# Performance work log

Hardware: AMD Instinct MI355X
Metric: run time of the kernel (lower is better)

The kernel has to match this reference:

```python
import jax, jax.numpy as jnp
import numpy as np

N = 50000   # nodes
E = 600000  # edges
D = 128     # emb_dim
L = 5       # num_layers
ATOM_DIMS = np.array([119, 4, 11, 13, 11, 7, 13, 2, 9]) + 5   # per-feature vocab (+5 as in source)
BOND_DIMS = np.array([7, 22, 2]) + 5
BL_CENTERS = np.arange(0.0, 2.0, 0.1, dtype=np.float32)   # 20 centers, gamma 10
PR_CENTERS = np.arange(0.0, 1.0, 0.05, dtype=np.float32)  # 20 centers, gamma 1
BL_GAMMA = 10.0
PR_GAMMA = 1.0
BN_EPS = 1e-5


def setup_inputs() -> dict:
    key = jax.random.key(0)
    ks = jax.random.split(key, 16)
    scale = 1.0 / np.sqrt(D)
    atom_off = jnp.asarray(np.concatenate([[0], np.cumsum(ATOM_DIMS)[:-1]]), jnp.int32)
    bond_off = jnp.asarray(np.concatenate([[0], np.cumsum(BOND_DIMS)[:-1]]), jnp.int32)
    return {
        "x": jax.random.randint(ks[0], (N, 9), 0, 7, dtype=jnp.int32),
        "edge_index": jax.random.randint(ks[1], (2, E), 0, N, dtype=jnp.int32),
        "edge_attr_int": jax.random.randint(ks[2], (E, 3), 0, 7, dtype=jnp.int32),
        "edge_attr_float": jax.random.uniform(ks[3], (E, 2), dtype=jnp.float32),
        "atom_off": atom_off,
        "bond_off": bond_off,
        "atom_emb": jax.random.normal(ks[4], (int(ATOM_DIMS.sum()), D), jnp.float32) * scale,
        "bond_emb": jax.random.normal(ks[5], (L, int(BOND_DIMS.sum()), D), jnp.float32) * scale,
        "W_bl": jax.random.normal(ks[6], (L, len(BL_CENTERS), D), jnp.float32) * scale,
        "b_bl": jnp.zeros((L, D), jnp.float32),
        "W_pr": jax.random.normal(ks[7], (L, len(PR_CENTERS), D), jnp.float32) * scale,
        "b_pr": jnp.zeros((L, D), jnp.float32),
        "mlp_W1": jax.random.normal(ks[8], (L, D, D), jnp.float32) * scale,
        "mlp_b1": jnp.zeros((L, D), jnp.float32),
        "bn1_g": jnp.ones((L, D), jnp.float32),
        "bn1_b": jnp.zeros((L, D), jnp.float32),
        "mlp_W2": jax.random.normal(ks[9], (L, D, D), jnp.float32) * scale,
        "mlp_b2": jnp.zeros((L, D), jnp.float32),
        "eps_gin": jnp.zeros((L,), jnp.float32),
        "bn_g": jnp.ones((L, D), jnp.float32),
        "bn_b": jnp.zeros((L, D), jnp.float32),
    }


def _bn(h, g, b):
    # BatchNorm1d, training-mode batch statistics over the node axis
    m = h.mean(0)
    v = h.var(0)
    return (h - m) * jax.lax.rsqrt(v + BN_EPS) * g + b


def _rbf(x, centers, gamma):
    # exp(-gamma * (x - c)^2): [E] -> [E, n_centers]
    return jnp.exp(-gamma * jnp.square(x[:, None] - centers[None, :]))


def reference(x, edge_index, edge_attr_int, edge_attr_float, atom_off, bond_off,
              atom_emb, bond_emb, W_bl, b_bl, W_pr, b_pr,
              mlp_W1, mlp_b1, bn1_g, bn1_b, mlp_W2, mlp_b2,
              eps_gin, bn_g, bn_b):
    # AtomEncoder: sum of 9 categorical embeddings (flat table + offsets)
    h = atom_emb[x + atom_off[None, :]].sum(1)  # [N, D]
    src, dst = edge_index[0], edge_index[1]
    bl = _rbf(edge_attr_float[:, 0], jnp.asarray(BL_CENTERS), BL_GAMMA)  # [E, 20]
    pr = _rbf(edge_attr_float[:, 1], jnp.asarray(PR_CENTERS), PR_GAMMA)  # [E, 20]
    for l in range(L):
        # per-layer edge embedding: BondEncoder + BondFloatRBF
        e = bond_emb[l][edge_attr_int + bond_off[None, :]].sum(1)
        e = e + bl @ W_bl[l] + b_bl[l] + pr @ W_pr[l] + b_pr[l]
        # GINConv (aggr='add'): mlp((1+eps)*x + sum_j relu(x_j + e_ij))
        msg = jax.nn.relu(h[src] + e)                       # [E, D]
        agg = jax.ops.segment_sum(msg, dst, num_segments=N)  # [N, D]
        z = (1.0 + eps_gin[l]) * h + agg
        z = z @ mlp_W1[l] + mlp_b1[l]
        z = jax.nn.relu(_bn(z, bn1_g[l], bn1_b[l]))
        z = z @ mlp_W2[l] + mlp_b2[l]
        # outer per-layer BatchNorm; ReLU except last layer (drop_ratio=0)
        z = _bn(z, bn_g[l], bn_b[l])
        if l < L - 1:
            z = jax.nn.relu(z)
        h = z
    return h  # JK='last'
```

## Files before the change

### kernel.cpp

```cpp
#include <hip/hip_runtime.h>
#include <hip/hip_bf16.h>

#define GN 50000
#define GE 600000
#define DD 128
#define TQ 4096
#define NBOND 2268
#define TROWS (2*(TQ+1) + NBOND)
#define SCB 49
#define NBANK 16
#define SSET (NBANK*256)
#define NB 782

typedef __attribute__((ext_vector_type(8))) short short8;
typedef __attribute__((ext_vector_type(4))) float floatx4;

__device__ __forceinline__ unsigned short f2b(float f) {
    __hip_bfloat16 h = __float2bfloat16(f);
    return __builtin_bit_cast(unsigned short, h);
}
__device__ __forceinline__ float b2f_lo(unsigned int u) { return __uint_as_float(u << 16); }
__device__ __forceinline__ float b2f_hi(unsigned int u) { return __uint_as_float(u & 0xffff0000u); }
__device__ __forceinline__ float bs2f(short s) {
    return __uint_as_float(((unsigned int)(unsigned short)s) << 16);
}

__global__ __launch_bounds__(256) void atom_kernel(
    const int* __restrict__ x, const int* __restrict__ atom_off,
    const float* __restrict__ atom_emb, unsigned short* __restrict__ h)
{
    int t = blockIdx.x * 256 + threadIdx.x;
    if (t >= GN * DD) return;
    int n = t >> 7, d = t & 127;
    float s = 0.f;
#pragma unroll
    for (int f = 0; f < 9; f++) {
        int idx = x[n * 9 + f] + atom_off[f];
        s += atom_emb[idx * DD + d];
    }
    h[t] = f2b(s);
}

__global__ __launch_bounds__(256) void hist_kernel(const int* __restrict__ ei, int* __restrict__ count)
{
    int e = blockIdx.x * 256 + threadIdx.x;
    if (e < GE) atomicAdd(&count[ei[GE + e]], 1);
}

__global__ __launch_bounds__(1024) void scan1_kernel(
    const int* __restrict__ count, int* __restrict__ row_start, int* __restrict__ blocksum)
{
    __shared__ int sh[1024];
    int t = threadIdx.x;
    int idx = blockIdx.x * 1024 + t;
    int v = (idx < GN) ? count[idx] : 0;
    sh[t] = v;
    __syncthreads();
    for (int off = 1; off < 1024; off <<= 1) {
        int u = (t >= off) ? sh[t - off] : 0;
        __syncthreads();
        sh[t] += u;
        __syncthreads();
    }
    if (idx <= GN) row_start[idx] = (t == 0) ? 0 : sh[t - 1];
    if (t == 1023) blocksum[blockIdx.x] = sh[1023];
}

__global__ __launch_bounds__(64) void scan2_kernel(
    const int* __restrict__ blocksum, int* __restrict__ blockoff)
{
    int t = threadIdx.x;
    int v = (t < SCB) ? blocksum[t] : 0;
#pragma unroll
    for (int off = 1; off < 64; off <<= 1) {
        int u = __shfl_up(v, off);
        if (t >= off) v += u;
    }
    int e = __shfl_up(v, 1);
    if (t == 0) e = 0;
    if (t < SCB) blockoff[t] = e;
}

__global__ __launch_bounds__(1024) void scan3_kernel(
    int* __restrict__ row_start, const int* __restrict__ blockoff)
{
    int idx = blockIdx.x * 1024 + threadIdx.x;
    if (idx <= GN) row_start[idx] += blockoff[blockIdx.x];
}

__global__ __launch_bounds__(256) void scatter_kernel(
    const int* __restrict__ ei, const int* __restrict__ eai, const float* __restrict__ eaf,
    const int* __restrict__ row_start, int* __restrict__ fill, int4* __restrict__ ep)
{
    int e = blockIdx.x * 256 + threadIdx.x;
    if (e < GE) {
        int d = ei[GE + e];
        int p = row_start[d] + atomicAdd(&fill[d], 1);
        int src = ei[e];
        float x1 = eaf[2 * e], x2 = eaf[2 * e + 1];
        int q1 = (int)(x1 * (float)TQ + 0.5f); q1 = min(max(q1, 0), TQ);
        int q2 = (int)(x2 * (float)TQ + 0.5f); q2 = min(max(q2, 0), TQ);
        int b0 = eai[3 * e], b1 = eai[3 * e + 1], b2 = eai[3 * e + 2];
        ep[p] = make_int4(src, q1 | (q2 << 16), (b0 * 27 + b1) * 7 + b2, 0);
    }
}

__global__ __launch_bounds__(128) void tables_kernel(
    const float* __restrict__ W_bl, const float* __restrict__ b_bl,
    const float* __restrict__ W_pr, const float* __restrict__ b_pr,
    const float* __restrict__ bond_emb, const int* __restrict__ bond_off,
    unsigned short* __restrict__ tbl_bl, unsigned short* __restrict__ tbl_pr,
    unsigned short* __restrict__ tbl_bond)
{
    int l = blockIdx.x / TROWS;
    int b = blockIdx.x % TROWS;
    int d = threadIdx.x;
    const float* W_bl_l = W_bl + (size_t)l * 20 * DD;
    const float* W_pr_l = W_pr + (size_t)l * 20 * DD;
    const float* bemb_l = bond_emb + (size_t)l * 46 * DD;
    if (b < (TQ + 1)) {
        float xq = b * (1.0f / TQ);
        float s = b_bl[(size_t)l * DD + d] + b_pr[(size_t)l * DD + d];
#pragma unroll
        for (int k = 0; k < 20; k++) {
            float dl = xq - 0.1f * k;
            s += __expf(-10.f * dl * dl) * W_bl_l[k * DD + d];
        }
        tbl_bl[((size_t)l * (TQ + 1) + b) * DD + d] = f2b(s);
    } else if (b < 2 * (TQ + 1)) {
        int q = b - (TQ + 1);
        float xq = q * (1.0f / TQ);
        float s = 0.f;
#pragma unroll
        for (int k = 0; k < 20; k++) {
            float dl = xq - 0.05f * k;
            s += __expf(-dl * dl) * W_pr_l[k * DD + d];
        }
        tbl_pr[((size_t)l * (TQ + 1) + q) * DD + d] = f2b(s);
    } else {
        int r = b - 2 * (TQ + 1);
        int b0 = r / 189;
        int rem = r % 189;
        int b1 = rem / 7, b2 = rem % 7;
        tbl_bond[((size_t)l * NBOND + r) * DD + d] =
            f2b(bemb_l[(b0 + bond_off[0]) * DD + d]
              + bemb_l[(b1 + bond_off[1]) * DD + d]
              + bemb_l[(b2 + bond_off[2]) * DD + d]);
    }
}

__global__ __launch_bounds__(256) void wfrag_kernel(
    const float* __restrict__ W1, const float* __restrict__ W2,
    unsigned short* __restrict__ wf_hi, unsigned short* __restrict__ wf_lo)
{
    int t = blockIdx.x * 256 + threadIdx.x;
    if (t >= 10 * 2048) return;
    int mat = t >> 11;
    int rem = t & 2047;
    int kt = rem >> 9;
    int rem2 = rem & 511;
    int nt = rem2 >> 6;
    int lane = rem2 & 63;
    const float* src = (mat & 1) ? (W2 + (size_t)(mat >> 1) * DD * DD)
                                 : (W1 + (size_t)(mat >> 1) * DD * DD);
    int n = nt * 16 + (lane & 15);
    int k0 = kt * 32 + (lane >> 4) * 8;
    size_t base = (size_t)mat * 16384 + (size_t)((kt * 8 + nt) * 64 + lane) * 8;
#pragma unroll
    for (int j = 0; j < 8; j++) {
        float w = src[(size_t)(k0 + j) * DD + n];
        unsigned short hi = f2b(w);
        wf_hi[base + j] = hi;
        wf_lo[base + j] = f2b(w - bs2f((short)hi));
    }
}

__global__ __launch_bounds__(256) void edge_kernel(
    const int4* __restrict__ ep,
    const unsigned short* __restrict__ tbl_bl, const unsigned short* __restrict__ tbl_pr,
    const unsigned short* __restrict__ tbl_bond,
    const unsigned short* __restrict__ hsrc, const int* __restrict__ row_start,
    const float* __restrict__ eps_gin, int layer, int apply_bn,
    const float* __restrict__ stats_prev, const float* __restrict__ g_prev,
    const float* __restrict__ b_prev,
    float* __restrict__ A)
{
    __shared__ float sc_s[DD], tr_s[DD];
    int tid = threadIdx.x;
    if (tid < DD) {
        float sc = 1.f, tr = 0.f;
        if (apply_bn) {
            float s = 0.f, q = 0.f;
#pragma unroll
            for (int bk = 0; bk < NBANK; bk++) {
                s += stats_prev[bk * 256 + tid];
                q += stats_prev[bk * 256 + 128 + tid];
            }
            float m = s * (1.0f / GN);
            float v = q * (1.0f / GN) - m * m;
            sc = g_prev[tid] * rsqrtf(v + 1e-5f);
            tr = b_prev[tid] - m * sc;
        }
        sc_s[tid] = sc;
        tr_s[tid] = tr;
    }
    __syncthreads();

    int wid = __builtin_amdgcn_readfirstlane(tid >> 6);
    int lane = tid & 63;
    float sc0 = sc_s[2 * lane],     tr0 = tr_s[2 * lane];
    float sc1 = sc_s[2 * lane + 1], tr1 = tr_s[2 * lane + 1];
    float rmin = apply_bn ? 0.f : -__builtin_inff();

    int n = blockIdx.x * 4 + wid;
    int s0 = __builtin_amdgcn_readfirstlane(row_start[n]);
    int s1 = __builtin_amdgcn_readfirstlane(row_start[n + 1]);
    const unsigned int* hu = (const unsigned int*)hsrc;
    const unsigned int* tb = (const unsigned int*)tbl_bl;
    const unsigned int* tp = (const unsigned int*)tbl_pr;
    const unsigned int* tg = (const unsigned int*)tbl_bond;
    float a0 = 0.f, a1 = 0.f;
    int p = s0;
    for (; p + 2 <= s1; p += 2) {
        int4 m0 = ep[p];
        int4 m1 = ep[p + 1];
        unsigned int ub0 = tb[(size_t)(m0.y & 0xffff) * 64 + lane];
        unsigned int up0 = tp[(size_t)((unsigned)m0.y >> 16) * 64 + lane];
        unsigned int ug0 = tg[(size_t)m0.z * 64 + lane];
        unsigned int uh0 = hu[(size_t)m0.x * 64 + lane];
        unsigned int ub1 = tb[(size_t)(m1.y & 0xffff) * 64 + lane];
        unsigned int up1 = tp[(size_t)((unsigned)m1.y >> 16) * 64 + lane];
        unsigned int ug1 = tg[(size_t)m1.z * 64 + lane];
        unsigned int uh1 = hu[(size_t)m1.x * 64 + lane];
        float h00 = fmaxf(fmaf(b2f_lo(uh0), sc0, tr0), rmin);
        float h01 = fmaxf(fmaf(b2f_hi(uh0), sc1, tr1), rmin);
        float h10 = fmaxf(fmaf(b2f_lo(uh1), sc0, tr0), rmin);
        float h11 = fmaxf(fmaf(b2f_hi(uh1), sc1, tr1), rmin);
        a0 += fmaxf(h00 + b2f_lo(ub0) + b2f_lo(up0) + b2f_lo(ug0), 0.f);
        a1 += fmaxf(h01 + b2f_hi(ub0) + b2f_hi(up0) + b2f_hi(ug0), 0.f);
        a0 += fmaxf(h10 + b2f_lo(ub1) + b2f_lo(up1) + b2f_lo(ug1), 0.f);
        a1 += fmaxf(h11 + b2f_hi(ub1) + b2f_hi(up1) + b2f_hi(ug1), 0.f);
    }
    if (p < s1) {
        int4 m0 = ep[p];
        unsigned int ub0 = tb[(size_t)(m0.y & 0xffff) * 64 + lane];
        unsigned int up0 = tp[(size_t)((unsigned)m0.y >> 16) * 64 + lane];
        unsigned int ug0 = tg[(size_t)m0.z * 64 + lane];
        unsigned int uh0 = hu[(size_t)m0.x * 64 + lane];
        float h00 = fmaxf(fmaf(b2f_lo(uh0), sc0, tr0), rmin);
        float h01 = fmaxf(fmaf(b2f_hi(uh0), sc1, tr1), rmin);
        a0 += fmaxf(h00 + b2f_lo(ub0) + b2f_lo(up0) + b2f_lo(ug0), 0.f);
        a1 += fmaxf(h01 + b2f_hi(ub0) + b2f_hi(up0) + b2f_hi(ug0), 0.f);
    }
    float eps1 = 1.f + eps_gin[layer];
    unsigned int un = hu[(size_t)n * 64 + lane];
    a0 += eps1 * fmaxf(fmaf(b2f_lo(un), sc0, tr0), rmin);
    a1 += eps1 * fmaxf(fmaf(b2f_hi(un), sc1, tr1), rmin);
    float2 o; o.x = a0; o.y = a1;
    *(float2*)(A + (size_t)n * DD + 2 * lane) = o;
}

__global__ __launch_bounds__(256) void gemm1_kernel(
    const float* __restrict__ Asrc,
    const unsigned short* __restrict__ wf_hi, const unsigned short* __restrict__ wf_lo,
    const float* __restrict__ bias, float* __restrict__ Cdst, float* __restrict__ stats_out)
{
    __shared__ float red_s[4][DD];
    __shared__ float red_q[4][DD];
    int tid = threadIdx.x, wid = tid >> 6, lane = tid & 63;
    int quad = lane >> 4, l16 = lane & 15;
    int row = blockIdx.x * 64 + wid * 16 + l16;
    bool rvalid = row < GN;

    floatx4 acc[8];
#pragma unroll
    for (int nt = 0; nt < 8; nt++) acc[nt] = (floatx4){0.f, 0.f, 0.f, 0.f};

    const short8* bhp = (const short8*)wf_hi;
    const short8* blp = (const short8*)wf_lo;
#pragma unroll
    for (int kt = 0; kt < 4; kt++) {
        short8 ahi = {0,0,0,0,0,0,0,0}, alo = {0,0,0,0,0,0,0,0};
        if (rvalid) {
            const float* ap = Asrc + (size_t)row * DD + kt * 32 + quad * 8;
            float a[8];
            *(float4*)(a)     = *(const float4*)(ap);
            *(float4*)(a + 4) = *(const float4*)(ap + 4);
#pragma unroll
            for (int j = 0; j < 8; j++) {
                unsigned short hi = f2b(a[j]);
                ahi[j] = (short)hi;
                alo[j] = (short)f2b(a[j] - bs2f((short)hi));
            }
        }
#pragma unroll
        for (int nt = 0; nt < 8; nt++) {
            short8 bhi = bhp[(kt * 8 + nt) * 64 + lane];
            short8 blo = blp[(kt * 8 + nt) * 64 + lane];
            acc[nt] = __builtin_amdgcn_mfma_f32_16x16x32_bf16(ahi, bhi, acc[nt], 0, 0, 0);
            acc[nt] = __builtin_amdgcn_mfma_f32_16x16x32_bf16(alo, bhi, acc[nt], 0, 0, 0);
            acc[nt] = __builtin_amdgcn_mfma_f32_16x16x32_bf16(ahi, blo, acc[nt], 0, 0, 0);
        }
    }

#pragma unroll
    for (int nt = 0; nt < 8; nt++) {
        int col = nt * 16 + l16;
        float bv = bias[col];
        float s = 0.f, q = 0.f;
#pragma unroll
        for (int v = 0; v < 4; v++) {
            int r = blockIdx.x * 64 + wid * 16 + quad * 4 + v;
            float o = acc[nt][v] + bv;
            if (r < GN) {
                s += o; q += o * o;
                Cdst[(size_t)r * DD + col] = o;
            }
        }
        s += __shfl_xor(s, 16); s += __shfl_xor(s, 32);
        q += __shfl_xor(q, 16); q += __shfl_xor(q, 32);
        if (lane < 16) { red_s[wid][col] = s; red_q[wid][col] = q; }
    }
    __syncthreads();
    int bank = blockIdx.x & (NBANK - 1);
    if (tid < DD) {
        float s = red_s[0][tid] + red_s[1][tid] + red_s[2][tid] + red_s[3][tid];
        atomicAdd(&stats_out[bank * 256 + tid], s);
    } else {
        int c = tid - DD;
        float q = red_q[0][c] + red_q[1][c] + red_q[2][c] + red_q[3][c];
        atomicAdd(&stats_out[bank * 256 + 128 + c], q);
    }
}

__global__ __launch_bounds__(256) void gemm2_kernel(
    const float* __restrict__ Asrc,
    const unsigned short* __restrict__ wf_hi, const unsigned short* __restrict__ wf_lo,
    const float* __restrict__ bias,
    unsigned short* __restrict__ Cbf, float* __restrict__ Cf32, int out_bf16,
    const float* __restrict__ stats_in, const float* __restrict__ bn_g,
    const float* __restrict__ bn_b, float* __restrict__ stats_out)
{
    __shared__ float sc_s[DD], tr_s[DD];
    __shared__ float red_s[4][DD];
    __shared__ float red_q[4][DD];
    int tid = threadIdx.x, wid = tid >> 6, lane = tid & 63;
    if (tid < DD) {
        float s = 0.f, q = 0.f;
#pragma unroll
        for (int bk = 0; bk < NBANK; bk++) {
            s += stats_in[bk * 256 + tid];
            q += stats_in[bk * 256 + 128 + tid];
        }
        float m = s * (1.0f / GN);
        float v = q * (1.0f / GN) - m * m;
        float sc = bn_g[tid] * rsqrtf(v + 1e-5f);
        sc_s[tid] = sc;
        tr_s[tid] = bn_b[tid] - m * sc;
    }
    __syncthreads();
    int quad = lane >> 4, l16 = lane & 15;
    int row = blockIdx.x * 64 + wid * 16 + l16;
    bool rvalid = row < GN;

    floatx4 acc[8];
#pragma unroll
    for (int nt = 0; nt < 8; nt++) acc[nt] = (floatx4){0.f, 0.f, 0.f, 0.f};

    const short8* bhp = (const short8*)wf_hi;
    const short8* blp = (const short8*)wf_lo;
#pragma unroll
    for (int kt = 0; kt < 4; kt++) {
        short8 ahi = {0,0,0,0,0,0,0,0}, alo = {0,0,0,0,0,0,0,0};
        if (rvalid) {
            const float* ap = Asrc + (size_t)row * DD + kt * 32 + quad * 8;
            float a[8];
            *(float4*)(a)     = *(const float4*)(ap);
            *(float4*)(a + 4) = *(const float4*)(ap + 4);
            int kb = kt * 32 + quad * 8;
#pragma unroll
            for (int j = 0; j < 8; j++)
                a[j] = fmaxf(a[j] * sc_s[kb + j] + tr_s[kb + j], 0.f);
#pragma unroll
            for (int j = 0; j < 8; j++) {
                unsigned short hi = f2b(a[j]);
                ahi[j] = (short)hi;
                alo[j] = (short)f2b(a[j] - bs2f((short)hi));
            }
        }
#pragma unroll
        for (int nt = 0; nt < 8; nt++) {
            short8 bhi = bhp[(kt * 8 + nt) * 64 + lane];
            short8 blo = blp[(kt * 8 + nt) * 64 + lane];
            acc[nt] = __builtin_amdgcn_mfma_f32_16x16x32_bf16(ahi, bhi, acc[nt], 0, 0, 0);
            acc[nt] = __builtin_amdgcn_mfma_f32_16x16x32_bf16(alo, bhi, acc[nt], 0, 0, 0);
            acc[nt] = __builtin_amdgcn_mfma_f32_16x16x32_bf16(ahi, blo, acc[nt], 0, 0, 0);
        }
    }

#pragma unroll
    for (int nt = 0; nt < 8; nt++) {
        int col = nt * 16 + l16;
        float bv = bias[col];
        float s = 0.f, q = 0.f;
#pragma unroll
        for (int v = 0; v < 4; v++) {
            int r = blockIdx.x * 64 + wid * 16 + quad * 4 + v;
            float o = acc[nt][v] + bv;
            if (r < GN) {
                s += o; q += o * o;
                if (out_bf16) Cbf[(size_t)r * DD + col] = f2b(o);
                else          Cf32[(size_t)r * DD + col] = o;
            }
        }
        s += __shfl_xor(s, 16); s += __shfl_xor(s, 32);
        q += __shfl_xor(q, 16); q += __shfl_xor(q, 32);
        if (lane < 16) { red_s[wid][col] = s; red_q[wid][col] = q; }
    }
    __syncthreads();
    int bank = blockIdx.x & (NBANK - 1);
    if (tid < DD) {
        float s = red_s[0][tid] + red_s[1][tid] + red_s[2][tid] + red_s[3][tid];
        atomicAdd(&stats_out[bank * 256 + tid], s);
    } else {
        int c = tid - DD;
        float q = red_q[0][c] + red_q[1][c] + red_q[2][c] + red_q[3][c];
        atomicAdd(&stats_out[bank * 256 + 128 + c], q);
    }
}

__global__ __launch_bounds__(256) void bn_apply_kernel(
    const float* __restrict__ Z, const float* __restrict__ stats2,
    const float* __restrict__ g, const float* __restrict__ b,
    float* __restrict__ fout)
{
    __shared__ float sc_s[DD], tr_s[DD];
    int tid = threadIdx.x;
    if (tid < DD) {
        float s = 0.f, q = 0.f;
#pragma unroll
        for (int bk = 0; bk < NBANK; bk++) {
            s += stats2[bk * 256 + tid];
            q += stats2[bk * 256 + 128 + tid];
        }
        float m = s * (1.0f / GN);
        float v = q * (1.0f / GN) - m * m;
        float sc = g[tid] * rsqrtf(v + 1e-5f);
        sc_s[tid] = sc;
        tr_s[tid] = b[tid] - m * sc;
    }
    __syncthreads();
    const int total = GN * DD;
    for (int t = blockIdx.x * 256 + tid; t < total; t += gridDim.x * 256) {
        int c = t & 127;
        fout[t] = Z[t] * sc_s[c] + tr_s[c];
    }
}

extern "C" void kernel_launch(void* const* d_in, const int* in_sizes, int n_in,
                              void* d_out, int out_size, void* d_ws, size_t ws_size,
                              hipStream_t stream)
{
    const int*   x        = (const int*)d_in[0];
    const int*   ei       = (const int*)d_in[1];
    const int*   eai      = (const int*)d_in[2];
    const float* eaf      = (const float*)d_in[3];
    const int*   atom_off = (const int*)d_in[4];
    const int*   bond_off = (const int*)d_in[5];
    const float* atom_emb = (const float*)d_in[6];
    const float* bond_emb = (const float*)d_in[7];
    const float* W_bl     = (const float*)d_in[8];
    const float* b_bl     = (const float*)d_in[9];
    const float* W_pr     = (const float*)d_in[10];
    const float* b_pr     = (const float*)d_in[11];
    const float* W1       = (const float*)d_in[12];
    const float* b1       = (const float*)d_in[13];
    const float* bn1g     = (const float*)d_in[14];
    const float* bn1b     = (const float*)d_in[15];
    const float* W2       = (const float*)d_in[16];
    const float* b2       = (const float*)d_in[17];
    const float* eps_gin  = (const float*)d_in[18];
    const float* bng      = (const float*)d_in[19];
    const float* bnb      = (const float*)d_in[20];
    float* out = (float*)d_out;

    char* p = (char*)d_ws;
    unsigned short* h_bf  = (unsigned short*)p;  p += (size_t)GN * DD * 2;
    unsigned short* z2_bf = (unsigned short*)p;  p += (size_t)GN * DD * 2;
    float* A              = (float*)p;           p += (size_t)GN * DD * 4;
    float* z1             = (float*)p;           p += (size_t)GN * DD * 4;
    float* z2f            = (float*)p;           p += (size_t)GN * DD * 4;
    unsigned short* tbl_bl   = (unsigned short*)p;  p += (size_t)5 * (TQ + 1) * DD * 2;
    unsigned short* tbl_pr   = (unsigned short*)p;  p += (size_t)5 * (TQ + 1) * DD * 2;
    unsigned short* tbl_bond = (unsigned short*)p;  p += (size_t)5 * NBOND * DD * 2;
    unsigned short* wf_hi    = (unsigned short*)p;  p += (size_t)10 * 16384 * 2;
    unsigned short* wf_lo    = (unsigned short*)p;  p += (size_t)10 * 16384 * 2;
    float* stats_all = (float*)p;  p += (size_t)10 * SSET * 4;
    int* count    = (int*)p;    p += (size_t)GN * 4;
    int* fill     = (int*)p;    p += (size_t)GN * 4;
    int* row_start= (int*)p;    p += (size_t)(GN + 1) * 4;
    int* blocksum = (int*)p;    p += (size_t)SCB * 4;
    int* blockoff = (int*)p;    p += (size_t)SCB * 4;
    p = (char*)(((size_t)p + 15) & ~(size_t)15);
    int4* ep      = (int4*)p;   p += (size_t)GE * 16;

    hipMemsetAsync(count, 0, (size_t)GN * 4, stream);
    hipMemsetAsync(fill,  0, (size_t)GN * 4, stream);
    hipMemsetAsync(stats_all, 0, (size_t)10 * SSET * 4, stream);

    hist_kernel<<<(GE + 255) / 256, 256, 0, stream>>>(ei, count);
    scan1_kernel<<<SCB, 1024, 0, stream>>>(count, row_start, blocksum);
    scan2_kernel<<<1, 64, 0, stream>>>(blocksum, blockoff);
    scan3_kernel<<<SCB, 1024, 0, stream>>>(row_start, blockoff);
    scatter_kernel<<<(GE + 255) / 256, 256, 0, stream>>>(ei, eai, eaf, row_start, fill, ep);
    atom_kernel<<<(GN * DD + 255) / 256, 256, 0, stream>>>(x, atom_off, atom_emb, h_bf);
    wfrag_kernel<<<80, 256, 0, stream>>>(W1, W2, wf_hi, wf_lo);
    tables_kernel<<<5 * TROWS, 128, 0, stream>>>(
        W_bl, b_bl, W_pr, b_pr, bond_emb, bond_off, tbl_bl, tbl_pr, tbl_bond);

    for (int l = 0; l < 5; l++) {
        float* stats1 = stats_all + (size_t)(2 * l + 0) * SSET;
        float* stats2 = stats_all + (size_t)(2 * l + 1) * SSET;
        float* stats2_prev = stats_all + (size_t)(2 * (l - 1) + 1) * SSET;

        edge_kernel<<<GN / 4, 256, 0, stream>>>(
            ep,
            tbl_bl + (size_t)l * (TQ + 1) * DD,
            tbl_pr + (size_t)l * (TQ + 1) * DD,
            tbl_bond + (size_t)l * NBOND * DD,
            (l == 0) ? h_bf : z2_bf, row_start, eps_gin, l,
            (l > 0) ? 1 : 0,
            (l > 0) ? stats2_prev : stats_all,
            bng + (size_t)(l > 0 ? l - 1 : 0) * DD,
            bnb + (size_t)(l > 0 ? l - 1 : 0) * DD,
            A);

        gemm1_kernel<<<NB, 256, 0, stream>>>(
            A, wf_hi + (size_t)(l * 2 + 0) * 16384, wf_lo + (size_t)(l * 2 + 0) * 16384,
            b1 + (size_t)l * DD, z1, stats1);

        gemm2_kernel<<<NB, 256, 0, stream>>>(
            z1, wf_hi + (size_t)(l * 2 + 1) * 16384, wf_lo + (size_t)(l * 2 + 1) * 16384,
            b2 + (size_t)l * DD,
            z2_bf, z2f, (l < 4) ? 1 : 0,
            stats1, bn1g + (size_t)l * DD, bn1b + (size_t)l * DD, stats2);
    }

    bn_apply_kernel<<<1024, 256, 0, stream>>>(
        z2f, stats_all + (size_t)9 * SSET, bng + (size_t)4 * DD, bnb + (size_t)4 * DD, out);
}
```

Baseline: 742.8 us.

## Split GEMM kernels across four column tiles to raise block count

Both MLP GEMM kernels now split the 128 output columns into four 32-column tiles, each handled by its own block, which quadruples the grid from 782 to 3128 blocks. The goal is more parallelism and fewer accumulator registers per thread, so occupancy rises and the 256 CUs are better filled. The cost is that every block re-reads and re-converts the same A rows to bf16 hi/lo, so A traffic and conversion work grow fourfold (mostly served from L2), and gemm2 recomputes the BN scale/shift in every block.

```diff
diff --git a/kernel.cpp b/kernel.cpp
--- a/kernel.cpp
+++ b/kernel.cpp
@@ -11,6 +11,7 @@
 #define NBANK 16
 #define SSET (NBANK*256)
 #define NB 782
+#define NB4 (NB*4)
 
 typedef __attribute__((ext_vector_type(8))) short short8;
 typedef __attribute__((ext_vector_type(4))) float floatx4;
@@ -265,16 +266,19 @@
     const unsigned short* __restrict__ wf_hi, const unsigned short* __restrict__ wf_lo,
     const float* __restrict__ bias, float* __restrict__ Cdst, float* __restrict__ stats_out)
 {
-    __shared__ float red_s[4][DD];
-    __shared__ float red_q[4][DD];
+    __shared__ float red_s[4][32];
+    __shared__ float red_q[4][32];
     int tid = threadIdx.x, wid = tid >> 6, lane = tid & 63;
+    int ct = blockIdx.x & 3;
+    int rb = blockIdx.x >> 2;
+    int row0 = rb * 64;
     int quad = lane >> 4, l16 = lane & 15;
-    int row = blockIdx.x * 64 + wid * 16 + l16;
+    int row = row0 + wid * 16 + l16;
     bool rvalid = row < GN;
 
-    floatx4 acc[8];
-#pragma unroll
-    for (int nt = 0; nt < 8; nt++) acc[nt] = (floatx4){0.f, 0.f, 0.f, 0.f};
+    floatx4 acc[2];
+    acc[0] = (floatx4){0.f, 0.f, 0.f, 0.f};
+    acc[1] = (floatx4){0.f, 0.f, 0.f, 0.f};
 
     const short8* bhp = (const short8*)wf_hi;
     const short8* blp = (const short8*)wf_lo;
@@ -294,9 +298,10 @@
             }
         }
 #pragma unroll
-        for (int nt = 0; nt < 8; nt++) {
-            short8 bhi = bhp[(kt * 8 + nt) * 64 + lane];
-            short8 blo = blp[(kt * 8 + nt) * 64 + lane];
+        for (int nt = 0; nt < 2; nt++) {
+            int ntg = ct * 2 + nt;
+            short8 bhi = bhp[(kt * 8 + ntg) * 64 + lane];
+            short8 blo = blp[(kt * 8 + ntg) * 64 + lane];
             acc[nt] = __builtin_amdgcn_mfma_f32_16x16x32_bf16(ahi, bhi, acc[nt], 0, 0, 0);
             acc[nt] = __builtin_amdgcn_mfma_f32_16x16x32_bf16(alo, bhi, acc[nt], 0, 0, 0);
             acc[nt] = __builtin_amdgcn_mfma_f32_16x16x32_bf16(ahi, blo, acc[nt], 0, 0, 0);
@@ -304,13 +309,13 @@
     }
 
 #pragma unroll
-    for (int nt = 0; nt < 8; nt++) {
-        int col = nt * 16 + l16;
+    for (int nt = 0; nt < 2; nt++) {
+        int col = (ct * 2 + nt) * 16 + l16;
         float bv = bias[col];
         float s = 0.f, q = 0.f;
 #pragma unroll
         for (int v = 0; v < 4; v++) {
-            int r = blockIdx.x * 64 + wid * 16 + quad * 4 + v;
+            int r = row0 + wid * 16 + quad * 4 + v;
             float o = acc[nt][v] + bv;
             if (r < GN) {
                 s += o; q += o * o;
@@ -319,17 +324,18 @@
         }
         s += __shfl_xor(s, 16); s += __shfl_xor(s, 32);
         q += __shfl_xor(q, 16); q += __shfl_xor(q, 32);
-        if (lane < 16) { red_s[wid][col] = s; red_q[wid][col] = q; }
+        if (lane < 16) { red_s[wid][nt * 16 + lane] = s; red_q[wid][nt * 16 + lane] = q; }
     }
     __syncthreads();
-    int bank = blockIdx.x & (NBANK - 1);
-    if (tid < DD) {
+    int bank = (blockIdx.x >> 2) & (NBANK - 1);
+    int c0 = ct * 32;
+    if (tid < 32) {
         float s = red_s[0][tid] + red_s[1][tid] + red_s[2][tid] + red_s[3][tid];
-        atomicAdd(&stats_out[bank * 256 + tid], s);
-    } else {
-        int c = tid - DD;
+        atomicAdd(&stats_out[bank * 256 + c0 + tid], s);
+    } else if (tid < 64) {
+        int c = tid - 32;
         float q = red_q[0][c] + red_q[1][c] + red_q[2][c] + red_q[3][c];
-        atomicAdd(&stats_out[bank * 256 + 128 + c], q);
+        atomicAdd(&stats_out[bank * 256 + 128 + c0 + c], q);
     }
 }
 
@@ -342,8 +348,8 @@
     const float* __restrict__ bn_b, float* __restrict__ stats_out)
 {
     __shared__ float sc_s[DD], tr_s[DD];
-    __shared__ float red_s[4][DD];
-    __shared__ float red_q[4][DD];
+    __shared__ float red_s[4][32];
+    __shared__ float red_q[4][32];
     int tid = threadIdx.x, wid = tid >> 6, lane = tid & 63;
     if (tid < DD) {
         float s = 0.f, q = 0.f;
@@ -359,13 +365,16 @@
         tr_s[tid] = bn_b[tid] - m * sc;
     }
     __syncthreads();
+    int ct = blockIdx.x & 3;
+    int rb = blockIdx.x >> 2;
+    int row0 = rb * 64;
     int quad = lane >> 4, l16 = lane & 15;
-    int row = blockIdx.x * 64 + wid * 16 + l16;
+    int row = row0 + wid * 16 + l16;
     bool rvalid = row < GN;
 
-    floatx4 acc[8];
-#pragma unroll
-    for (int nt = 0; nt < 8; nt++) acc[nt] = (floatx4){0.f, 0.f, 0.f, 0.f};
+    floatx4 acc[2];
+    acc[0] = (floatx4){0.f, 0.f, 0.f, 0.f};
+    acc[1] = (floatx4){0.f, 0.f, 0.f, 0.f};
 
     const short8* bhp = (const short8*)wf_hi;
     const short8* blp = (const short8*)wf_lo;
@@ -389,9 +398,10 @@
             }
         }
 #pragma unroll
-        for (int nt = 0; nt < 8; nt++) {
-            short8 bhi = bhp[(kt * 8 + nt) * 64 + lane];
-            short8 blo = blp[(kt * 8 + nt) * 64 + lane];
+        for (int nt = 0; nt < 2; nt++) {
+            int ntg = ct * 2 + nt;
+            short8 bhi = bhp[(kt * 8 + ntg) * 64 + lane];
+            short8 blo = blp[(kt * 8 + ntg) * 64 + lane];
             acc[nt] = __builtin_amdgcn_mfma_f32_16x16x32_bf16(ahi, bhi, acc[nt], 0, 0, 0);
             acc[nt] = __builtin_amdgcn_mfma_f32_16x16x32_bf16(alo, bhi, acc[nt], 0, 0, 0);
             acc[nt] = __builtin_amdgcn_mfma_f32_16x16x32_bf16(ahi, blo, acc[nt], 0, 0, 0);
@@ -399,13 +409,13 @@
     }
 
 #pragma unroll
-    for (int nt = 0; nt < 8; nt++) {
-        int col = nt * 16 + l16;
+    for (int nt = 0; nt < 2; nt++) {
+        int col = (ct * 2 + nt) * 16 + l16;
         float bv = bias[col];
         float s = 0.f, q = 0.f;
 #pragma unroll
         for (int v = 0; v < 4; v++) {
-            int r = blockIdx.x * 64 + wid * 16 + quad * 4 + v;
+            int r = row0 + wid * 16 + quad * 4 + v;
             float o = acc[nt][v] + bv;
             if (r < GN) {
                 s += o; q += o * o;
@@ -415,17 +425,18 @@
         }
         s += __shfl_xor(s, 16); s += __shfl_xor(s, 32);
         q += __shfl_xor(q, 16); q += __shfl_xor(q, 32);
-        if (lane < 16) { red_s[wid][col] = s; red_q[wid][col] = q; }
+        if (lane < 16) { red_s[wid][nt * 16 + lane] = s; red_q[wid][nt * 16 + lane] = q; }
     }
     __syncthreads();
-    int bank = blockIdx.x & (NBANK - 1);
-    if (tid < DD) {
+    int bank = (blockIdx.x >> 2) & (NBANK - 1);
+    int c0 = ct * 32;
+    if (tid < 32) {
         float s = red_s[0][tid] + red_s[1][tid] + red_s[2][tid] + red_s[3][tid];
-        atomicAdd(&stats_out[bank * 256 + tid], s);
-    } else {
-        int c = tid - DD;
+        atomicAdd(&stats_out[bank * 256 + c0 + tid], s);
+    } else if (tid < 64) {
+        int c = tid - 32;
         float q = red_q[0][c] + red_q[1][c] + red_q[2][c] + red_q[3][c];
-        atomicAdd(&stats_out[bank * 256 + 128 + c], q);
+        atomicAdd(&stats_out[bank * 256 + 128 + c0 + c], q);
     }
 }
 
@@ -535,11 +546,11 @@
             bnb + (size_t)(l > 0 ? l - 1 : 0) * DD,
             A);
 
-        gemm1_kernel<<<NB, 256, 0, stream>>>(
+        gemm1_kernel<<<NB4, 256, 0, stream>>>(
             A, wf_hi + (size_t)(l * 2 + 0) * 16384, wf_lo + (size_t)(l * 2 + 0) * 16384,
             b1 + (size_t)l * DD, z1, stats1);
 
-        gemm2_kernel<<<NB, 256, 0, stream>>>(
+        gemm2_kernel<<<NB4, 256, 0, stream>>>(
             z1, wf_hi + (size_t)(l * 2 + 1) * 16384, wf_lo + (size_t)(l * 2 + 1) * 16384,
             b2 + (size_t)l * DD,
             z2_bf, z2f, (l < 4) ? 1 : 0,
```

Result: no change. 747.8 us (+0.7%).

## Stage GEMM A tile in LDS and split output columns across waves

Applied to the files above, without the earlier changes.

The two MLP GEMM kernels are merged into one template. Each block now loads its 64-row A tile into padded shared memory with coalesced float4 loads. Each wave then computes all 64 rows for 2 of the 8 column tiles, so each wave fetches a quarter of the hi/lo weight fragments it fetched before, and the A rows are reused across its MFMAs. The per-block shared reduction of BN statistics is replaced by per-wave atomics straight into the banked stats buffer. The cost is 4x more global atomics, an extra LDS round trip, and an unguarded tile load that reads past row N in the last block.

```diff
diff --git a/kernel.cpp b/kernel.cpp
--- a/kernel.cpp
+++ b/kernel.cpp
@@ -11,6 +11,7 @@
 #define NBANK 16
 #define SSET (NBANK*256)
 #define NB 782
+#define LDA2 132
 
 typedef __attribute__((ext_vector_type(8))) short short8;
 typedef __attribute__((ext_vector_type(4))) float floatx4;
@@ -260,80 +261,8 @@
     *(float2*)(A + (size_t)n * DD + 2 * lane) = o;
 }
 
-__global__ __launch_bounds__(256) void gemm1_kernel(
-    const float* __restrict__ Asrc,
-    const unsigned short* __restrict__ wf_hi, const unsigned short* __restrict__ wf_lo,
-    const float* __restrict__ bias, float* __restrict__ Cdst, float* __restrict__ stats_out)
-{
-    __shared__ float red_s[4][DD];
-    __shared__ float red_q[4][DD];
-    int tid = threadIdx.x, wid = tid >> 6, lane = tid & 63;
-    int quad = lane >> 4, l16 = lane & 15;
-    int row = blockIdx.x * 64 + wid * 16 + l16;
-    bool rvalid = row < GN;
-
-    floatx4 acc[8];
-#pragma unroll
-    for (int nt = 0; nt < 8; nt++) acc[nt] = (floatx4){0.f, 0.f, 0.f, 0.f};
-
-    const short8* bhp = (const short8*)wf_hi;
-    const short8* blp = (const short8*)wf_lo;
-#pragma unroll
-    for (int kt = 0; kt < 4; kt++) {
-        short8 ahi = {0,0,0,0,0,0,0,0}, alo = {0,0,0,0,0,0,0,0};
-        if (rvalid) {
-            const float* ap = Asrc + (size_t)row * DD + kt * 32 + quad * 8;
-            float a[8];
-            *(float4*)(a)     = *(const float4*)(ap);
-            *(float4*)(a + 4) = *(const float4*)(ap + 4);
-#pragma unroll
-            for (int j = 0; j < 8; j++) {
-                unsigned short hi = f2b(a[j]);
-                ahi[j] = (short)hi;
-                alo[j] = (short)f2b(a[j] - bs2f((short)hi));
-            }
-        }
-#pragma unroll
-        for (int nt = 0; nt < 8; nt++) {
-            short8 bhi = bhp[(kt * 8 + nt) * 64 + lane];
-            short8 blo = blp[(kt * 8 + nt) * 64 + lane];
-            acc[nt] = __builtin_amdgcn_mfma_f32_16x16x32_bf16(ahi, bhi, acc[nt], 0, 0, 0);
-            acc[nt] = __builtin_amdgcn_mfma_f32_16x16x32_bf16(alo, bhi, acc[nt], 0, 0, 0);
-            acc[nt] = __builtin_amdgcn_mfma_f32_16x16x32_bf16(ahi, blo, acc[nt], 0, 0, 0);
-        }
-    }
-
-#pragma unroll
-    for (int nt = 0; nt < 8; nt++) {
-        int col = nt * 16 + l16;
-        float bv = bias[col];
-        float s = 0.f, q = 0.f;
-#pragma unroll
-        for (int v = 0; v < 4; v++) {
-            int r = blockIdx.x * 64 + wid * 16 + quad * 4 + v;
-            float o = acc[nt][v] + bv;
-            if (r < GN) {
-                s += o; q += o * o;
-                Cdst[(size_t)r * DD + col] = o;
-            }
-        }
-        s += __shfl_xor(s, 16); s += __shfl_xor(s, 32);
-        q += __shfl_xor(q, 16); q += __shfl_xor(q, 32);
-        if (lane < 16) { red_s[wid][col] = s; red_q[wid][col] = q; }
-    }
-    __syncthreads();
-    int bank = blockIdx.x & (NBANK - 1);
-    if (tid < DD) {
-        float s = red_s[0][tid] + red_s[1][tid] + red_s[2][tid] + red_s[3][tid];
-        atomicAdd(&stats_out[bank * 256 + tid], s);
-    } else {
-        int c = tid - DD;
-        float q = red_q[0][c] + red_q[1][c] + red_q[2][c] + red_q[3][c];
-        atomicAdd(&stats_out[bank * 256 + 128 + c], q);
-    }
-}
-
-__global__ __launch_bounds__(256) void gemm2_kernel(
+template <int MODE>
+__global__ __launch_bounds__(256) void gemm_kernel(
     const float* __restrict__ Asrc,
     const unsigned short* __restrict__ wf_hi, const unsigned short* __restrict__ wf_lo,
     const float* __restrict__ bias,
@@ -341,91 +270,109 @@
     const float* __restrict__ stats_in, const float* __restrict__ bn_g,
     const float* __restrict__ bn_b, float* __restrict__ stats_out)
 {
+    __shared__ float At[64 * LDA2];
     __shared__ float sc_s[DD], tr_s[DD];
-    __shared__ float red_s[4][DD];
-    __shared__ float red_q[4][DD];
     int tid = threadIdx.x, wid = tid >> 6, lane = tid & 63;
-    if (tid < DD) {
-        float s = 0.f, q = 0.f;
-#pragma unroll
-        for (int bk = 0; bk < NBANK; bk++) {
-            s += stats_in[bk * 256 + tid];
-            q += stats_in[bk * 256 + 128 + tid];
-        }
-        float m = s * (1.0f / GN);
-        float v = q * (1.0f / GN) - m * m;
-        float sc = bn_g[tid] * rsqrtf(v + 1e-5f);
-        sc_s[tid] = sc;
-        tr_s[tid] = bn_b[tid] - m * sc;
+    int row0 = blockIdx.x * 64;
+
+    if (MODE == 1) {
+        if (tid < DD) {
+            float s = 0.f, q = 0.f;
+#pragma unroll
+            for (int bk = 0; bk < NBANK; bk++) {
+                s += stats_in[bk * 256 + tid];
+                q += stats_in[bk * 256 + 128 + tid];
+            }
+            float m = s * (1.0f / GN);
+            float v = q * (1.0f / GN) - m * m;
+            float sc = bn_g[tid] * rsqrtf(v + 1e-5f);
+            sc_s[tid] = sc;
+            tr_s[tid] = bn_b[tid] - m * sc;
+        }
+    }
+
+    {
+        const float* g = Asrc + (size_t)row0 * DD;
+#pragma unroll
+        for (int i = 0; i < 8; i++) {
+            int idx = i * 1024 + tid * 4;
+            float4 v = *(const float4*)(g + idx);
+            int r = idx >> 7, c = idx & 127;
+            *(float4*)(At + r * LDA2 + c) = v;
+        }
     }
     __syncthreads();
+
     int quad = lane >> 4, l16 = lane & 15;
-    int row = blockIdx.x * 64 + wid * 16 + l16;
-    bool rvalid = row < GN;
-
-    floatx4 acc[8];
-#pragma unroll
-    for (int nt = 0; nt < 8; nt++) acc[nt] = (floatx4){0.f, 0.f, 0.f, 0.f};
+    floatx4 acc[4][2];
+#pragma unroll
+    for (int rt = 0; rt < 4; rt++)
+#pragma unroll
+        for (int nt = 0; nt < 2; nt++) acc[rt][nt] = (floatx4){0.f, 0.f, 0.f, 0.f};
 
     const short8* bhp = (const short8*)wf_hi;
     const short8* blp = (const short8*)wf_lo;
 #pragma unroll
     for (int kt = 0; kt < 4; kt++) {
-        short8 ahi = {0,0,0,0,0,0,0,0}, alo = {0,0,0,0,0,0,0,0};
-        if (rvalid) {
-            const float* ap = Asrc + (size_t)row * DD + kt * 32 + quad * 8;
+        short8 ahi[4], alo[4];
+        int kb = kt * 32 + quad * 8;
+#pragma unroll
+        for (int rt = 0; rt < 4; rt++) {
+            const float* ap = At + (rt * 16 + l16) * LDA2 + kb;
             float a[8];
             *(float4*)(a)     = *(const float4*)(ap);
             *(float4*)(a + 4) = *(const float4*)(ap + 4);
-            int kb = kt * 32 + quad * 8;
-#pragma unroll
-            for (int j = 0; j < 8; j++)
-                a[j] = fmaxf(a[j] * sc_s[kb + j] + tr_s[kb + j], 0.f);
+            if (MODE == 1) {
+#pragma unroll
+                for (int j = 0; j < 8; j++)
+                    a[j] = fmaxf(a[j] * sc_s[kb + j] + tr_s[kb + j], 0.f);
+            }
 #pragma unroll
             for (int j = 0; j < 8; j++) {
                 unsigned short hi = f2b(a[j]);
-                ahi[j] = (short)hi;
-                alo[j] = (short)f2b(a[j] - bs2f((short)hi));
-            }
-        }
-#pragma unroll
-        for (int nt = 0; nt < 8; nt++) {
-            short8 bhi = bhp[(kt * 8 + nt) * 64 + lane];
-            short8 blo = blp[(kt * 8 + nt) * 64 + lane];
-            acc[nt] = __builtin_amdgcn_mfma_f32_16x16x32_bf16(ahi, bhi, acc[nt], 0, 0, 0);
-            acc[nt] = __builtin_amdgcn_mfma_f32_16x16x32_bf16(alo, bhi, acc[nt], 0, 0, 0);
-            acc[nt] = __builtin_amdgcn_mfma_f32_16x16x32_bf16(ahi, blo, acc[nt], 0, 0, 0);
-        }
-    }
-
-#pragma unroll
-    for (int nt = 0; nt < 8; nt++) {
-        int col = nt * 16 + l16;
+                ahi[rt][j] = (short)hi;
+                alo[rt][j] = (short)f2b(a[j] - bs2f((short)hi));
+            }
+        }
+#pragma unroll
+        for (int nt = 0; nt < 2; nt++) {
+            int ntg = wid * 2 + nt;
+            short8 bhi = bhp[(kt * 8 + ntg) * 64 + lane];
+            short8 blo = blp[(kt * 8 + ntg) * 64 + lane];
+#pragma unroll
+            for (int rt = 0; rt < 4; rt++) {
+                acc[rt][nt] = __builtin_amdgcn_mfma_f32_16x16x32_bf16(ahi[rt], bhi, acc[rt][nt], 0, 0, 0);
+                acc[rt][nt] = __builtin_amdgcn_mfma_f32_16x16x32_bf16(alo[rt], bhi, acc[rt][nt], 0, 0, 0);
+                acc[rt][nt] = __builtin_amdgcn_mfma_f32_16x16x32_bf16(ahi[rt], blo, acc[rt][nt], 0, 0, 0);
+            }
+        }
+    }
+
+    int bank = blockIdx.x & (NBANK - 1);
+#pragma unroll
+    for (int nt = 0; nt < 2; nt++) {
+        int col = (wid * 2 + nt) * 16 + l16;
         float bv = bias[col];
         float s = 0.f, q = 0.f;
 #pragma unroll
-        for (int v = 0; v < 4; v++) {
-            int r = blockIdx.x * 64 + wid * 16 + quad * 4 + v;
-            float o = acc[nt][v] + bv;
-            if (r < GN) {
-                s += o; q += o * o;
-                if (out_bf16) Cbf[(size_t)r * DD + col] = f2b(o);
-                else          Cf32[(size_t)r * DD + col] = o;
+        for (int rt = 0; rt < 4; rt++) {
+#pragma unroll
+            for (int v = 0; v < 4; v++) {
+                int r = row0 + rt * 16 + quad * 4 + v;
+                float o = acc[rt][nt][v] + bv;
+                if (r < GN) {
+                    s += o; q += o * o;
+                    if (MODE == 1 && out_bf16) Cbf[(size_t)r * DD + col] = f2b(o);
+                    else                       Cf32[(size_t)r * DD + col] = o;
+                }
             }
         }
         s += __shfl_xor(s, 16); s += __shfl_xor(s, 32);
         q += __shfl_xor(q, 16); q += __shfl_xor(q, 32);
-        if (lane < 16) { red_s[wid][col] = s; red_q[wid][col] = q; }
-    }
-    __syncthreads();
-    int bank = blockIdx.x & (NBANK - 1);
-    if (tid < DD) {
-        float s = red_s[0][tid] + red_s[1][tid] + red_s[2][tid] + red_s[3][tid];
-        atomicAdd(&stats_out[bank * 256 + tid], s);
-    } else {
-        int c = tid - DD;
-        float q = red_q[0][c] + red_q[1][c] + red_q[2][c] + red_q[3][c];
-        atomicAdd(&stats_out[bank * 256 + 128 + c], q);
+        if (lane < 16) {
+            atomicAdd(&stats_out[bank * 256 + col], s);
+            atomicAdd(&stats_out[bank * 256 + 128 + col], q);
+        }
     }
 }
 
@@ -535,14 +482,14 @@
             bnb + (size_t)(l > 0 ? l - 1 : 0) * DD,
             A);
 
-        gemm1_kernel<<<NB, 256, 0, stream>>>(
+        gemm_kernel<0><<<NB, 256, 0, stream>>>(
             A, wf_hi + (size_t)(l * 2 + 0) * 16384, wf_lo + (size_t)(l * 2 + 0) * 16384,
-            b1 + (size_t)l * DD, z1, stats1);
-
-        gemm2_kernel<<<NB, 256, 0, stream>>>(
+            b1 + (size_t)l * DD, nullptr, z1, 0,
+            nullptr, nullptr, nullptr, stats1);
+
+        gemm_kernel<1><<<NB, 256, 0, stream>>>(
             z1, wf_hi + (size_t)(l * 2 + 1) * 16384, wf_lo + (size_t)(l * 2 + 1) * 16384,
-            b2 + (size_t)l * DD,
-            z2_bf, z2f, (l < 4) ? 1 : 0,
+            b2 + (size_t)l * DD, z2_bf, z2f, (l < 4) ? 1 : 0,
             stats1, bn1g + (size_t)l * DD, bn1b + (size_t)l * DD, stats2);
     }
 
```

Result: faster. 692.7 us (-6.7%).
